# Performance work log

Hardware: AMD Instinct MI355X
Metric: run time of the kernel (lower is better)

## Reference

```python
import jax, jax.numpy as jnp
import numpy as np
from jax import lax

HEADS = 8
DIM_HEAD = 64
NUM_LANDMARKS = 256
PINV_ITERS = 6
CONV_PAD = 33 // 2  # 16


def moore_penrose_pinv(x, iters):
    # x: [..., m, m]
    abs_x = jnp.abs(x)
    col = abs_x.sum(-1).max()
    row = abs_x.sum(-2).max()
    z = jnp.swapaxes(x, -1, -2) / (col * row)
    I = jnp.eye(x.shape[-1], dtype=x.dtype)
    for _ in range(iters):
        xz = x @ z
        z = 0.25 * (z @ (13.0 * I - xz @ (15.0 * I - xz @ (7.0 * I - xz))))
    return z


def setup_inputs() -> dict:
    key = jax.random.key(0)
    k1, k2, k3, k4, k5 = jax.random.split(key, 5)
    b, n, dim = 4, 4096, 512
    inner = HEADS * DIM_HEAD
    return {
        "x": jax.random.normal(k1, (b, n, dim), jnp.float32),
        "w_qkv": jax.random.normal(k2, (dim, 3 * inner), jnp.float32) * 0.02,
        "w_out": jax.random.normal(k3, (inner, dim), jnp.float32) * 0.02,
        "b_out": jax.random.normal(k4, (dim,), jnp.float32) * 0.02,
        "res_kernel": jax.random.normal(k5, (HEADS, 1, 33, 1), jnp.float32) * 0.1,
    }


def reference(x, w_qkv, w_out, b_out, res_kernel):
    b, n, dim = x.shape
    h, dh, m = HEADS, DIM_HEAD, NUM_LANDMARKS
    scale = dh ** -0.5
    # n chosen as a multiple of m, so the pad branch is a no-op.
    l = n // m  # tokens per landmark group

    qkv = x @ w_qkv  # [b, n, 3*h*dh]
    q, k, v = jnp.split(qkv, 3, axis=-1)
    to_heads = lambda t: t.reshape(b, n, h, dh).transpose(0, 2, 1, 3)  # [b,h,n,dh]
    q, k, v = to_heads(q), to_heads(k), to_heads(v)
    q = q * scale

    # landmarks: mean over consecutive groups of l tokens
    q_l = q.reshape(b, h, m, l, dh).sum(3) / l  # [b,h,m,dh]
    k_l = k.reshape(b, h, m, l, dh).sum(3) / l

    attn1 = jax.nn.softmax(jnp.einsum("bhnd,bhmd->bhnm", q, k_l), axis=-1)  # [b,h,n,m]
    attn2 = jax.nn.softmax(jnp.einsum("bhid,bhjd->bhij", q_l, k_l), axis=-1)  # [b,h,m,m]
    attn3 = jax.nn.softmax(jnp.einsum("bhmd,bhnd->bhmn", q_l, k), axis=-1)  # [b,h,m,n]

    attn2_pinv = moore_penrose_pinv(attn2, PINV_ITERS)
    out = (attn1 @ attn2_pinv) @ (attn3 @ v)  # [b,h,n,dh]

    # depthwise residual conv over the sequence dim (Conv2d(h, h, (33,1), groups=h))
    res = lax.conv_general_dilated(
        v, res_kernel, window_strides=(1, 1),
        padding=((CONV_PAD, CONV_PAD), (0, 0)),
        dimension_numbers=("NCHW", "OIHW", "NCHW"),
        feature_group_count=h,
    )
    out = out + res

    out = out.transpose(0, 2, 1, 3).reshape(b, n, h * dh)
    out = out @ w_out + b_out
    return out
```

## Files before the change

### kernel.cpp

```cpp
#include <hip/hip_runtime.h>

#define Nq   4096
#define DHq  64
#define Mq   256
#define BHq  32

using bf16 = __bf16;
using bf16x8 = __bf16 __attribute__((ext_vector_type(8)));
using bf16x4 = __bf16 __attribute__((ext_vector_type(4)));
using f32x4 = float __attribute__((ext_vector_type(4)));

__device__ __forceinline__ f32x4 mfma16(bf16x8 a, bf16x8 b, f32x4 c) {
  return __builtin_amdgcn_mfma_f32_16x16x32_bf16(a, b, c, 0, 0, 0);
}
__device__ __forceinline__ unsigned short f2bu(float f) {
  bf16 b = (bf16)f;
  return __builtin_bit_cast(unsigned short, b);
}
__device__ __forceinline__ void split_store(bf16* h, bf16* l, long idx, float v) {
  bf16 hi = (bf16)v;
  h[idx] = hi;
  l[idx] = (bf16)(v - (float)hi);
}

typedef const __attribute__((address_space(1))) void* gas_t;
typedef __attribute__((address_space(3))) void* las_t;
__device__ __forceinline__ void glds16(const bf16* g, bf16* l) {
  __builtin_amdgcn_global_load_lds((gas_t)g, (las_t)l, 16, 0, 0);
}

template<int ROWS, int SRC>
__device__ __forceinline__ void stageA(const void* src, long ld, long row0, int k0,
                                       bf16* dst, int t) {
#pragma unroll
  for (int c = 0; c < ROWS / 64; ++c) {
    int idx = t + 256 * c;
    int r = idx >> 2;
    int kc = (idx & 3) << 3;
    bf16x8 val;
    if constexpr (SRC == 0) {
      val = *(const bf16x8*)((const bf16*)src + (row0 + r) * ld + k0 + kc);
    } else {
      const float* s = (const float*)src + (row0 + r) * ld + k0 + kc;
      float4 a = *(const float4*)s;
      float4 b = *(const float4*)(s + 4);
      val[0]=(bf16)a.x; val[1]=(bf16)a.y; val[2]=(bf16)a.z; val[3]=(bf16)a.w;
      val[4]=(bf16)b.x; val[5]=(bf16)b.y; val[6]=(bf16)b.z; val[7]=(bf16)b.w;
    }
    *(bf16x8*)(dst + r * 40 + kc) = val;
  }
}

template<int COLS, bool F32>
__device__ __forceinline__ void stageBN(const void* src, long ld, long n0, int k0,
                                        unsigned int* dst, int t) {
  int kp = t >> 4;
  int nb = (t & 15) << 2;
#pragma unroll
  for (int g = 0; g < COLS / 64; ++g) {
    int n = nb + (g << 6);
    unsigned int w0, w1, w2, w3;
    if constexpr (F32) {
      const float* s0 = (const float*)src + (long)(k0 + 2 * kp) * ld + n0 + n;
      const float* s1 = s0 + ld;
      float4 a = *(const float4*)s0;
      float4 b = *(const float4*)s1;
      w0 = f2bu(a.x) | ((unsigned)f2bu(b.x) << 16);
      w1 = f2bu(a.y) | ((unsigned)f2bu(b.y) << 16);
      w2 = f2bu(a.z) | ((unsigned)f2bu(b.z) << 16);
      w3 = f2bu(a.w) | ((unsigned)f2bu(b.w) << 16);
    } else {
      const unsigned short* s0 = (const unsigned short*)src + (long)(k0 + 2 * kp) * ld + n0 + n;
      const unsigned short* s1 = s0 + ld;
      ushort4 a = *(const ushort4*)s0;
      ushort4 b = *(const ushort4*)s1;
      w0 = a.x | ((unsigned)b.x << 16);
      w1 = a.y | ((unsigned)b.y << 16);
      w2 = a.z | ((unsigned)b.z << 16);
      w3 = a.w | ((unsigned)b.w << 16);
    }
    dst[(n + 0) * 20 + kp] = w0;
    dst[(n + 1) * 20 + kp] = w1;
    dst[(n + 2) * 20 + kp] = w2;
    dst[(n + 3) * 20 + kp] = w3;
  }
}

#define EQKV 0
#define EA2 1
#define EWT 8
#define EBIAS 9

struct GP {
  const void* A; const void* Al;
  const void* B; const void* Bl;
  long ldA, ldB, sA, sB;
  int K;
  void* C0; void* C1; void* C2;
  long sC, ldC;
  const void* x0; const void* x1;
  const float* bias;
};

template<int BM, int BN, int WX, int ASRC, int BMODE, int SPLIT, int EPI, int SWZ>
__global__ __launch_bounds__(256, 2) void mgemm(GP p) {
  constexpr int WY = 4 / WX;
  constexpr int TM = BM / WY, TN = BN / WX;
  constexpr int IT = TM / 16, JT = TN / 16;
  constexpr int AB = (SPLIT ? 2 : 1) * BM * 80;
  constexpr int BB = (SPLIT ? 2 : 1) * BN * 80;
  __shared__ __align__(16) char Lbuf[AB + BB];
  bf16* AsL = (bf16*)Lbuf;
  unsigned int* BsL = (unsigned int*)(Lbuf + AB);
  int t = threadIdx.x;
  int wv = t >> 6, lane = t & 63;
  int wy = wv / WX, wx = wv % WX;
  int qd = lane >> 4, lm = lane & 15;
  long bz = blockIdx.z, m0 = (long)blockIdx.y * BM, n0 = (long)blockIdx.x * BN;

  const void* Ap = (const bf16*)p.A + bz * p.sA;
  const void* Alp = nullptr;
  if constexpr (SPLIT) Alp = (const bf16*)p.Al + bz * p.sA;
  const void* Bp = (const bf16*)p.B + bz * p.sB;
  const void* Blp = nullptr;
  if constexpr (SPLIT) Blp = (const bf16*)p.Bl + bz * p.sB;

  f32x4 acc[IT][JT];
#pragma unroll
  for (int i = 0; i < IT; ++i)
#pragma unroll
    for (int j = 0; j < JT; ++j) acc[i][j] = (f32x4)0.0f;

  for (int k0 = 0; k0 < p.K; k0 += 32) {
    stageA<BM, ASRC>(Ap, p.ldA, m0, k0, AsL, t);
    if constexpr (SPLIT) stageA<BM, 0>(Alp, p.ldA, m0, k0, AsL + BM * 40, t);
    if constexpr (BMODE == 0) {
      stageA<BN, 0>(Bp, p.ldB, n0, k0, (bf16*)BsL, t);
      if constexpr (SPLIT) stageA<BN, 0>(Blp, p.ldB, n0, k0, (bf16*)BsL + BN * 40, t);
    } else {
      stageBN<BN, false>(Bp, p.ldB, n0, k0, BsL, t);
      if constexpr (SPLIT) stageBN<BN, false>(Blp, p.ldB, n0, k0, BsL + BN * 20, t);
    }
    __syncthreads();
    bf16x8 af[IT], afl[IT];
#pragma unroll
    for (int i = 0; i < IT; ++i) {
      int m = wy * TM + i * 16 + lm;
      af[i] = *(const bf16x8*)(AsL + m * 40 + qd * 8);
      if constexpr (SPLIT) afl[i] = *(const bf16x8*)(AsL + BM * 40 + m * 40 + qd * 8);
    }
#pragma unroll
    for (int j = 0; j < JT; ++j) {
      int n = wx * TN + j * 16 + lm;
      bf16x8 bf, bfl;
      if constexpr (BMODE == 0) {
        bf = *(const bf16x8*)((const bf16*)BsL + n * 40 + qd * 8);
        if constexpr (SPLIT) bfl = *(const bf16x8*)((const bf16*)BsL + BN * 40 + n * 40 + qd * 8);
      } else {
        bf = *(const bf16x8*)((const bf16*)(BsL + n * 20 + qd * 4));
        if constexpr (SPLIT) bfl = *(const bf16x8*)((const bf16*)(BsL + BN * 20 + n * 20 + qd * 4));
      }
#pragma unroll
      for (int i = 0; i < IT; ++i) {
        acc[i][j] = mfma16(af[i], bf, acc[i][j]);
        if constexpr (SPLIT) {
          acc[i][j] = mfma16(af[i], bfl, acc[i][j]);
          acc[i][j] = mfma16(afl[i], bf, acc[i][j]);
        }
      }
    }
    __syncthreads();
  }

  if constexpr (EPI == EA2) {
#pragma unroll
    for (int r = 0; r < 4; ++r) {
      long row = m0 + wy * TM + qd * 4 + r;
      float e[JT];
      float s = 0.f;
#pragma unroll
      for (int j = 0; j < JT; ++j) { e[j] = __expf(acc[0][j][r]); s += e[j]; }
      s += __shfl_xor(s, 1); s += __shfl_xor(s, 2);
      s += __shfl_xor(s, 4); s += __shfl_xor(s, 8);
      float inv = 1.0f / s;
#pragma unroll
      for (int j = 0; j < JT; ++j) {
        long col = n0 + j * 16 + lm;
        split_store((bf16*)p.C0, (bf16*)p.C1, bz * p.sC + row * p.ldC + col, e[j] * inv);
      }
    }
  } else {
#pragma unroll
    for (int i = 0; i < IT; ++i)
#pragma unroll
      for (int j = 0; j < JT; ++j)
#pragma unroll
        for (int r = 0; r < 4; ++r) {
          long row = m0 + wy * TM + i * 16 + qd * 4 + r;
          long col = n0 + wx * TN + j * 16 + lm;
          float v = acc[i][j][r];
          if constexpr (EPI == EWT) {
            ((bf16*)p.C0)[bz * 16384 + col * 256 + row] = (bf16)v;
          }
        }
  }
}

template<int ASRC, int EPI, int SWZ>
__global__ __launch_bounds__(256, 3) void ggemm(GP p) {
  __shared__ __align__(64) bf16 AsL[2][128 * 32];
  __shared__ __align__(64) bf16 BsL[2][128 * 32];
  int t = threadIdx.x, wv = t >> 6, lane = t & 63;
  int wy = wv >> 1, wx = wv & 1;
  int qd = lane >> 4, lm = lane & 15;
  long m0, n0;
  if constexpr (SWZ == 1) {
    int b = blockIdx.x, xcd = b & 7, s = b >> 3;
    m0 = (long)(xcd * 16 + s / 12) * 128; n0 = (long)(s % 12) * 128;
  } else {
    int b = blockIdx.x, xcd = b & 7, s = b >> 3;
    m0 = (long)(xcd * 16 + (s >> 2)) * 128; n0 = (long)(s & 3) * 128;
  }
  const bf16* A = (const bf16*)p.A;
  const bf16* B = (const bf16*)p.B;

  f32x4 acc[4][4];
#pragma unroll
  for (int i = 0; i < 4; ++i)
#pragma unroll
    for (int j = 0; j < 4; ++j) acc[i][j] = (f32x4)0.0f;

  int rsub = lane >> 2;
  int kc = (lane & 3) << 3;
  for (int k0 = 0; k0 < p.K; k0 += 64) {
#pragma unroll
    for (int half = 0; half < 2; ++half) {
      int kk = k0 + half * 32;
#pragma unroll
      for (int e = 0; e < 2; ++e) {
        int br = wv * 32 + e * 16;
        long rA = m0 + br + rsub;
        const bf16* gA;
        if constexpr (ASRC == 0) {
          gA = A + rA * p.ldA + kk + kc;
        } else {
          long bb = rA >> 12, ii = rA & 4095;
          int k = kk + kc;
          long h = k >> 6, d = k & 63;
          gA = A + (((bb * 8 + h) * 4096 + ii) * 64 + d);
        }
        glds16(gA, AsL[half] + br * 32);
        const bf16* gB = B + (n0 + br + rsub) * p.ldB + kk + kc;
        glds16(gB, BsL[half] + br * 32);
      }
    }
    __syncthreads();
#pragma unroll
    for (int half = 0; half < 2; ++half) {
      bf16x8 af[4];
#pragma unroll
      for (int i = 0; i < 4; ++i)
        af[i] = *(const bf16x8*)(AsL[half] + (wy * 64 + i * 16 + lm) * 32 + qd * 8);
#pragma unroll
      for (int j = 0; j < 4; ++j) {
        bf16x8 bv = *(const bf16x8*)(BsL[half] + (wx * 64 + j * 16 + lm) * 32 + qd * 8);
#pragma unroll
        for (int i = 0; i < 4; ++i) acc[i][j] = mfma16(af[i], bv, acc[i][j]);
      }
    }
    __syncthreads();
  }

#pragma unroll
  for (int i = 0; i < 4; ++i)
#pragma unroll
    for (int j = 0; j < 4; ++j)
#pragma unroll
      for (int r = 0; r < 4; ++r) {
        long row = m0 + wy * 64 + i * 16 + qd * 4 + r;
        long col = n0 + wx * 64 + j * 16 + lm;
        float v = acc[i][j][r];
        if constexpr (EPI == EQKV) {
          int part = (int)(col >> 9);
          long h = (col >> 6) & 7, d = col & 63;
          long bb = row >> 12, ii = row & 4095;
          float scv = part == 0 ? 0.125f : 1.0f;
          bf16* dst = part == 0 ? (bf16*)p.C0 : (part == 1 ? (bf16*)p.C1 : (bf16*)p.C2);
          dst[((bb * 8 + h) * 4096 + ii) * 64 + d] = (bf16)(v * scv);
        } else {
          ((float*)p.C0)[row * 512 + col] = v + p.bias[col];
        }
      }
}

__global__ __launch_bounds__(256) void k_prep(const float* __restrict__ x,
                                              bf16* __restrict__ xb,
                                              float* a3vf, float* rs3, unsigned int* sc) {
  long i = (long)blockIdx.x * 256 + threadIdx.x;
  long e = i * 8;
  float4 a = *(const float4*)(x + e);
  float4 b = *(const float4*)(x + e + 4);
  bf16x8 v;
  v[0]=(bf16)a.x; v[1]=(bf16)a.y; v[2]=(bf16)a.z; v[3]=(bf16)a.w;
  v[4]=(bf16)b.x; v[5]=(bf16)b.y; v[6]=(bf16)b.z; v[7]=(bf16)b.w;
  *(bf16x8*)(xb + e) = v;
  if (i < 524288) a3vf[i] = 0.f;
  if (i < 8192) rs3[i] = 0.f;
  if (i == 0) sc[0] = 0u;
}

__global__ __launch_bounds__(256) void k_wtrans2(const float* __restrict__ wq,
                                                 const float* __restrict__ wo,
                                                 bf16* __restrict__ wqt,
                                                 bf16* __restrict__ wot) {
  __shared__ float T[64][65];
  int bx = blockIdx.x, ti = blockIdx.y;
  const float* src; bf16* dst; int N, tj;
  if (bx < 24) { src = wq; dst = wqt; N = 1536; tj = bx; }
  else         { src = wo; dst = wot; N = 512;  tj = bx - 24; }
  int t = threadIdx.x;
  int c = t & 63, r0 = t >> 6;
#pragma unroll
  for (int rr = 0; rr < 16; ++rr) {
    int r = r0 * 16 + rr;
    T[r][c] = src[(long)(ti * 64 + r) * N + tj * 64 + c];
  }
  __syncthreads();
#pragma unroll
  for (int rr = 0; rr < 16; ++rr) {
    int n = r0 * 16 + rr;
    dst[(long)(tj * 64 + n) * 512 + ti * 64 + c] = (bf16)T[c][n];
  }
}

#define SBW 132

__device__ __forceinline__ void stageBS32(const bf16* src, long n0, int k0,
                                          unsigned int* dst, int t) {
  int kp = t >> 3, nb = (t & 7) << 2;
  const unsigned short* s0 = (const unsigned short*)src + (long)(k0 + 2 * kp) * 256 + n0 + nb;
  const unsigned short* s1 = s0 + 256;
  ushort4 a = *(const ushort4*)s0;
  ushort4 b = *(const ushort4*)s1;
  int wb = (k0 >> 1) + kp;
  dst[(nb + 0) * SBW + wb] = a.x | ((unsigned)b.x << 16);
  dst[(nb + 1) * SBW + wb] = a.y | ((unsigned)b.y << 16);
  dst[(nb + 2) * SBW + wb] = a.z | ((unsigned)b.z << 16);
  dst[(nb + 3) * SBW + wb] = a.w | ((unsigned)b.w << 16);
}

template<int SPLIT>
__device__ __forceinline__ void sgemm32(const bf16* Ah, const bf16* Al,
                                        const unsigned int* Bs, const unsigned int* Bsl,
                                        int w, int lane, f32x4 acc[2]) {
  int qd = lane >> 4, lm = lane & 15;
  acc[0] = (f32x4)0.0f;
  acc[1] = (f32x4)0.0f;
#pragma unroll 2
  for (int k0 = 0; k0 < 256; k0 += 32) {
    long m = w * 16 + lm;
    bf16x8 af = *(const bf16x8*)(Ah + m * 256 + k0 + qd * 8);
    bf16x8 afl;
    if constexpr (SPLIT) afl = *(const bf16x8*)(Al + m * 256 + k0 + qd * 8);
#pragma unroll
    for (int j = 0; j < 2; ++j) {
      bf16x8 bv = *(const bf16x8*)((const bf16*)(Bs + (j * 16 + lm) * SBW + (k0 >> 1) + qd * 4));
      acc[j] = mfma16(af, bv, acc[j]);
      if constexpr (SPLIT) {
        bf16x8 bl = *(const bf16x8*)((const bf16*)(Bsl + (j * 16 + lm) * SBW + (k0 >> 1) + qd * 4));
        acc[j] = mfma16(af, bl, acc[j]);
        acc[j] = mfma16(afl, bv, acc[j]);
      }
    }
  }
}

template<int HASL>
__device__ __forceinline__ void packStrip(unsigned int* Sh, unsigned int* Sl,
                                          int col, int R0, const float* v) {
  unsigned int* Wp = Sh + col * SBW + (R0 >> 1);
  Wp[0] = f2bu(v[0]) | ((unsigned)f2bu(v[1]) << 16);
  Wp[1] = f2bu(v[2]) | ((unsigned)f2bu(v[3]) << 16);
  if constexpr (HASL) {
    unsigned int* Wq = Sl + col * SBW + (R0 >> 1);
    Wq[0] = f2bu(v[0] - (float)(bf16)v[0]) | ((unsigned)f2bu(v[1] - (float)(bf16)v[1]) << 16);
    Wq[1] = f2bu(v[2] - (float)(bf16)v[2]) | ((unsigned)f2bu(v[3] - (float)(bf16)v[3]) << 16);
  }
}

__device__ __forceinline__ void nsmap(int b, long& bh, long& js) {
  int xcd = b & 7, s = b >> 3;
  bh = xcd * 4 + (s >> 3);
  js = (long)(s & 7) * 32;
}

__global__ __launch_bounds__(1024) void k_nsy0(const bf16* __restrict__ A2h,
                                               const bf16* __restrict__ zh,
                                               bf16* __restrict__ yh, bf16* __restrict__ yl) {
  __shared__ __align__(16) unsigned int Bs[32 * SBW];
  int b = blockIdx.x, t = threadIdx.x;
  long bh, js;
  nsmap(b, bh, js);
  const bf16* Ah = A2h + bh * 65536;
  const bf16* Bz = zh + bh * 65536;
  if (t < 128) {
#pragma unroll
    for (int k0 = 0; k0 < 256; k0 += 32) stageBS32(Bz, js, k0, Bs, t);
  }
  __syncthreads();
  int w = t >> 6, lane = t & 63, qd = lane >> 4, lm = lane & 15;
  f32x4 acc[2];
  sgemm32<0>(Ah, Ah, Bs, Bs, w, lane, acc);
  bf16* yhb = yh + bh * 65536;
  bf16* ylb = yl + bh * 65536;
#pragma unroll
  for (int j = 0; j < 2; ++j)
#pragma unroll
    for (int r = 0; r < 4; ++r) {
      long row = w * 16 + qd * 4 + r;
      long col = js + j * 16 + lm;
      split_store(yhb, ylb, row * 256 + col, acc[j][r]);
    }
}

template<int SPLIT, int YS>
__global__ __launch_bounds__(1024) void k_ns4(
    const bf16* __restrict__ A2h, const bf16* __restrict__ A2l,
    const bf16* __restrict__ yih, const bf16* __restrict__ yil,
    const bf16* __restrict__ zh_, const bf16* __restrict__ zl_,
    bf16* __restrict__ znh_, bf16* __restrict__ znl_,
    bf16* __restrict__ yoh_, bf16* __restrict__ yol_) {
  constexpr int P0 = SPLIT ? 2 : 1;
  constexpr int P1 = (SPLIT || YS == 1) ? 2 : 1;
  __shared__ __align__(16) unsigned int S0[P0][32 * SBW];
  __shared__ __align__(16) unsigned int S1[P1][32 * SBW];
  int b = blockIdx.x, t = threadIdx.x;
  long bh, js;
  nsmap(b, bh, js);
  const bf16* yH = yih + bh * 65536;
  const bf16* yL = yil + bh * 65536;
  const bf16* zH = zh_ + bh * 65536;
  const bf16* zL = zl_ + bh * 65536;
  const bf16* aH = A2h + bh * 65536;
  const bf16* aL = A2l + bh * 65536;
  unsigned int* S0l = S0[P0 - 1];
  unsigned int* S1l = S1[P1 - 1];
  if (t < 128) {
#pragma unroll
    for (int k0 = 0; k0 < 256; k0 += 32) {
      stageBS32(yH, js, k0, S0[0], t);
      if constexpr (SPLIT) stageBS32(yL, js, k0, S0l, t);
    }
  }
  __syncthreads();
  int w = t >> 6, lane = t & 63, qd = lane >> 4, lm = lane & 15;
  f32x4 acc[2];

  sgemm32<SPLIT>(yH, yL, S0[0], S0l, w, lane, acc);
#pragma unroll
  for (int j = 0; j < 2; ++j) {
    int R0 = w * 16 + qd * 4;
    int col = j * 16 + lm;
    float v[4];
#pragma unroll
    for (int r = 0; r < 4; ++r) {
      long row = R0 + r;
      long ix = row * 256 + js + col;
      float yv = (float)yH[ix] + (float)yL[ix];
      v[r] = ((row == js + col) ? 15.0f : 0.0f) - 7.0f * yv + acc[j][r];
    }
    packStrip<SPLIT>(S1[0], S1l, col, R0, v);
  }
  __syncthreads();

  sgemm32<SPLIT>(yH, yL, S1[0], S1l, w, lane, acc);
#pragma unroll
  for (int j = 0; j < 2; ++j) {
    int R0 = w * 16 + qd * 4;
    int col = j * 16 + lm;
    float v[4];
#pragma unroll
    for (int r = 0; r < 4; ++r)
      v[r] = (((long)(R0 + r) == js + col) ? 13.0f : 0.0f) - acc[j][r];
    packStrip<SPLIT>(S0[0], S0l, col, R0, v);
  }
  __syncthreads();

  sgemm32<SPLIT>(zH, zL, S0[0], S0l, w, lane, acc);
  bf16* zoh = znh_ + bh * 65536;
  bf16* zol = znl_ + bh * 65536;
#pragma unroll
  for (int j = 0; j < 2; ++j) {
    int R0 = w * 16 + qd * 4;
    int col = j * 16 + lm;
    float v[4];
#pragma unroll
    for (int r = 0; r < 4; ++r) {
      v[r] = 0.25f * acc[j][r];
      split_store(zoh, zol, (long)(R0 + r) * 256 + js + col, v[r]);
    }
    if constexpr (YS >= 0) packStrip<(YS == 1) ? 1 : 0>(S1[0], S1l, col, R0, v);
  }

  if constexpr (YS >= 0) {
    __syncthreads();
    sgemm32<(YS == 1) ? 1 : 0>(aH, aL, S1[0], S1l, w, lane, acc);
    bf16* yoh = yoh_ + bh * 65536;
    bf16* yol = yol_ + bh * 65536;
#pragma unroll
    for (int j = 0; j < 2; ++j)
#pragma unroll
      for (int r = 0; r < 4; ++r) {
        long row = w * 16 + qd * 4 + r;
        long col = js + j * 16 + lm;
        split_store(yoh, yol, row * 256 + col, acc[j][r]);
      }
  }
}

__device__ __forceinline__ void loadKrow4(const bf16* ks_, int t, bf16x8 kr[4]) {
#pragma unroll
  for (int c = 0; c < 4; ++c) {
    int idx = t + 256 * c;
    int r = idx >> 3, dc = (idx & 7) * 8;
    kr[c] = *(const bf16x8*)(ks_ + r * 64 + dc);
  }
}
__device__ __forceinline__ void writeKrow4(bf16* kS, int t, const bf16x8 kr[4]) {
#pragma unroll
  for (int c = 0; c < 4; ++c) {
    int idx = t + 256 * c;
    int r = idx >> 3, dc = (idx & 7) * 8;
    *(bf16x8*)(kS + r * 72 + dc) = kr[c];
  }
}
__device__ __forceinline__ void loadVhalf(const bf16* vs_, int k0, int t,
                                          ushort4& a, ushort4& b) {
  int kp = t >> 4, nb = (t & 15) << 2;
  const unsigned short* s0 = (const unsigned short*)vs_ + (long)(k0 + 2 * kp) * 64 + nb;
  a = *(const ushort4*)s0;
  b = *(const ushort4*)(s0 + 64);
}
__device__ __forceinline__ void writeVhalf(unsigned int* dst, int t, ushort4 a, ushort4 b) {
  int kp = t >> 4, nb = (t & 15) << 2;
  dst[(nb + 0) * 20 + kp] = a.x | ((unsigned)b.x << 16);
  dst[(nb + 1) * 20 + kp] = a.y | ((unsigned)b.y << 16);
  dst[(nb + 2) * 20 + kp] = a.z | ((unsigned)b.z << 16);
  dst[(nb + 3) * 20 + kp] = a.w | ((unsigned)b.w << 16);
}

__global__ __launch_bounds__(256, 2) void k_a3v(const bf16* __restrict__ qlh,
                                                const bf16* __restrict__ kb,
                                                const bf16* __restrict__ vb,
                                                float* __restrict__ a3vf,
                                                float* __restrict__ rs3) {
  __shared__ __align__(16) char L[66048];
  bf16* qlS = (bf16*)L;
  bf16* kS  = (bf16*)(L + 9216);
  bf16* PA  = (bf16*)(L + 27648);
  unsigned int* vBb = (unsigned int*)(L + 45056);
  float* rsL = (float*)(L + 65536);
  int b = blockIdx.x, t = threadIdx.x;
  int xcd = b & 7, s = b >> 3;
  int strip = xcd * 16 + (s >> 2);
  int qt = s & 3;
  long bz = strip >> 2;
  int kt = strip & 3;
  int wv = t >> 6, lane = t & 63, qd = lane >> 4, lm = lane & 15;
  int wy = wv >> 1, wx = wv & 1;
  const bf16* qlp = qlh + bz * 16384 + qt * 64 * 64;
#pragma unroll
  for (int c = 0; c < 2; ++c) {
    int idx = t + 256 * c;
    int r = idx >> 3, dc = (idx & 7) * 8;
    *(bf16x8*)(qlS + r * 72 + dc) = *(const bf16x8*)(qlp + r * 64 + dc);
  }
  const bf16* kb_ = kb + bz * 262144 + (long)kt * 65536;
  const bf16* vb_ = vb + bz * 262144 + (long)kt * 65536;
  f32x4 accO[2][2];
  float rsum[2][4];
#pragma unroll
  for (int i = 0; i < 2; ++i) {
#pragma unroll
    for (int j = 0; j < 2; ++j) accO[i][j] = (f32x4)0.0f;
#pragma unroll
    for (int r = 0; r < 4; ++r) rsum[i][r] = 0.f;
  }
  bf16x8 kr[4];
  ushort4 va[4], vbq[4];
  loadKrow4(kb_, t, kr);
#pragma unroll
  for (int q = 0; q < 4; ++q) loadVhalf(vb_, q * 32, t, va[q], vbq[q]);
  for (int tt = 0; tt < 8; ++tt) {
    __syncthreads();
    writeKrow4(kS, t, kr);
#pragma unroll
    for (int q = 0; q < 4; ++q) writeVhalf(vBb + q * 1280, t, va[q], vbq[q]);
    __syncthreads();
    if (tt < 7) {
      const bf16* ks2 = kb_ + (tt + 1) * 8192;
      const bf16* vs2 = vb_ + (tt + 1) * 8192;
      loadKrow4(ks2, t, kr);
#pragma unroll
      for (int q = 0; q < 4; ++q) loadVhalf(vs2, q * 32, t, va[q], vbq[q]);
    }
    f32x4 s2[2][4];
#pragma unroll
    for (int i = 0; i < 2; ++i)
#pragma unroll
      for (int j = 0; j < 4; ++j) s2[i][j] = (f32x4)0.0f;
#pragma unroll
    for (int ks = 0; ks < 2; ++ks) {
      bf16x8 af[2];
#pragma unroll
      for (int i = 0; i < 2; ++i)
        af[i] = *(const bf16x8*)(qlS + (wy * 32 + i * 16 + lm) * 72 + ks * 32 + qd * 8);
#pragma unroll
      for (int j = 0; j < 4; ++j) {
        bf16x8 bfv = *(const bf16x8*)(kS + (wx * 64 + j * 16 + lm) * 72 + ks * 32 + qd * 8);
#pragma unroll
        for (int i = 0; i < 2; ++i) s2[i][j] = mfma16(af[i], bfv, s2[i][j]);
      }
    }
#pragma unroll
    for (int i = 0; i < 2; ++i)
#pragma unroll
      for (int r = 0; r < 4; ++r) {
        int row = wy * 32 + i * 16 + qd * 4 + r;
        float cs = 0.f;
#pragma unroll
        for (int j = 0; j < 4; ++j) {
          float e = __expf(s2[i][j][r]);
          PA[row * 136 + wx * 64 + j * 16 + lm] = (bf16)e;
          cs += e;
        }
        cs += __shfl_xor(cs, 1); cs += __shfl_xor(cs, 2);
        cs += __shfl_xor(cs, 4); cs += __shfl_xor(cs, 8);
        rsum[i][r] += cs;
      }
    __syncthreads();
#pragma unroll
    for (int ks = 0; ks < 4; ++ks) {
      const unsigned int* vB = vBb + ks * 1280;
      bf16x8 af[2];
#pragma unroll
      for (int i = 0; i < 2; ++i)
        af[i] = *(const bf16x8*)(PA + (wy * 32 + i * 16 + lm) * 136 + ks * 32 + qd * 8);
#pragma unroll
      for (int j = 0; j < 2; ++j) {
        bf16x8 bfv = *(const bf16x8*)((const bf16*)(vB + (wx * 32 + j * 16 + lm) * 20) + qd * 8);
#pragma unroll
        for (int i = 0; i < 2; ++i) accO[i][j] = mfma16(af[i], bfv, accO[i][j]);
      }
    }
  }
  if (lm == 0) {
#pragma unroll
    for (int i = 0; i < 2; ++i)
#pragma unroll
      for (int r = 0; r < 4; ++r)
        rsL[(wy * 32 + i * 16 + qd * 4 + r) * 2 + wx] = rsum[i][r];
  }
  __syncthreads();
  if (t < 64) atomicAdd(&rs3[bz * 256 + qt * 64 + t], rsL[t * 2] + rsL[t * 2 + 1]);
#pragma unroll
  for (int i = 0; i < 2; ++i)
#pragma unroll
    for (int j = 0; j < 2; ++j)
#pragma unroll
      for (int r = 0; r < 4; ++r) {
        long row = bz * 256 + qt * 64 + wy * 32 + i * 16 + qd * 4 + r;
        long col = wx * 32 + j * 16 + lm;
        atomicAdd(&a3vf[row * 64 + col], accO[i][j][r]);
      }
}

__global__ void k_a3vnorm(const float* __restrict__ a3vf, const float* __restrict__ rs3,
                          bf16* __restrict__ a3vh, bf16* __restrict__ a3vl) {
  long e0 = ((long)blockIdx.x * 256 + threadIdx.x) * 4;
  float4 vv = *(const float4*)&a3vf[e0];
  float inv = 1.0f / rs3[e0 >> 6];
  split_store(a3vh, a3vl, e0 + 0, vv.x * inv);
  split_store(a3vh, a3vl, e0 + 1, vv.y * inv);
  split_store(a3vh, a3vl, e0 + 2, vv.z * inv);
  split_store(a3vh, a3vl, e0 + 3, vv.w * inv);
}

__global__ void k_landmarks(const bf16* q, const bf16* k, bf16* qlh, bf16* qll,
                            bf16* klh, bf16* kll) {
  int bm = blockIdx.x;
  int bh = bm >> 8, mi = bm & 255;
  int d = threadIdx.x;
  const bf16* qp = q + ((long)bh * 4096 + mi * 16) * 64 + d;
  const bf16* kp = k + ((long)bh * 4096 + mi * 16) * 64 + d;
  float sq = 0.f, sk = 0.f;
#pragma unroll
  for (int tt = 0; tt < 16; ++tt) { sq += (float)qp[tt * 64]; sk += (float)kp[tt * 64]; }
  sq *= 0.0625f; sk *= 0.0625f;
  long o = (long)bh * 16384 + mi * 64 + d;
  split_store(qlh, qll, o, sq);
  split_store(klh, kll, o, sk);
}

__global__ __launch_bounds__(256) void k_colsum(const bf16* A2h, const bf16* A2l,
                                                unsigned int* sc) {
  int bh = blockIdx.x, j = threadIdx.x;
  const bf16* ph = A2h + (long)bh * 65536 + j;
  const bf16* pl = A2l + (long)bh * 65536 + j;
  float s = 0.f;
  for (int i = 0; i < 256; ++i) s += (float)ph[i * 256] + (float)pl[i * 256];
  __shared__ float red[256];
  red[j] = s; __syncthreads();
  for (int o = 128; o > 0; o >>= 1) {
    if (j < o) red[j] = fmaxf(red[j], red[j + o]);
    __syncthreads();
  }
  if (j == 0) atomicMax(sc, __float_as_uint(red[0]));
}

__global__ __launch_bounds__(256) void k_zinit(const bf16* A2h, const bf16* A2l,
                                               const unsigned int* sc, bf16* zh, bf16* zl) {
  __shared__ float T[64][65];
  int bh = blockIdx.z, ti = blockIdx.y, tj = blockIdx.x;
  int t = threadIdx.x;
  int c = t & 63, r0 = t >> 6;
  long base = (long)bh * 65536;
  float inv = 1.0f / __uint_as_float(sc[0]);
#pragma unroll
  for (int rr = 0; rr < 16; ++rr) {
    int r = r0 * 16 + rr;
    long idx = base + (long)(ti * 64 + r) * 256 + tj * 64 + c;
    T[r][c] = (float)A2h[idx] + (float)A2l[idx];
  }
  __syncthreads();
#pragma unroll
  for (int rr = 0; rr < 16; ++rr) {
    int jl = r0 * 16 + rr;
    float v = T[c][jl] * inv;
    long o = base + (long)(tj * 64 + jl) * 256 + ti * 64 + c;
    split_store(zh, zl, o, v);
  }
}

__global__ __launch_bounds__(256, 2) void k_attn1w(const bf16* qb, const bf16* klb,
                                                   const bf16* Wt, bf16* oh) {
  __shared__ __align__(16) char L[38912];
  bf16* Aq = (bf16*)L;
  bf16* Bkl = (bf16*)(L + 5120);
  bf16* Pl = (bf16*)L;
  bf16* Bw = (bf16*)(L + 33792);
  int t = threadIdx.x, wv = t >> 6, lane = t & 63;
  int qd = lane >> 4, lm = lane & 15;
  long bz = blockIdx.z;
  long m0 = (long)blockIdx.x * 64;
  const bf16* qA = qb + bz * (4096L * 64);
  const bf16* klA = klb + bz * (256L * 64);
  const bf16* WtA = Wt + bz * 16384;

  f32x4 a1[16];
#pragma unroll
  for (int j = 0; j < 16; ++j) a1[j] = (f32x4)0.0f;
  for (int k0 = 0; k0 < 64; k0 += 32) {
    stageA<64, 0>(qA, 64, m0, k0, Aq, t);
    stageA<256, 0>(klA, 64, 0, k0, Bkl, t);
    __syncthreads();
    bf16x8 af = *(const bf16x8*)(Aq + (wv * 16 + lm) * 40 + qd * 8);
#pragma unroll
    for (int j = 0; j < 16; ++j) {
      bf16x8 bf = *(const bf16x8*)(Bkl + (j * 16 + lm) * 40 + qd * 8);
      a1[j] = mfma16(af, bf, a1[j]);
    }
    __syncthreads();
  }
  float rs[4];
#pragma unroll
  for (int r = 0; r < 4; ++r) {
    int rowl = wv * 16 + qd * 4 + r;
    float ev[16];
    float s = 0.f;
#pragma unroll
    for (int j = 0; j < 16; ++j) { ev[j] = __expf(a1[j][r]); s += ev[j]; }
    s += __shfl_xor(s, 1); s += __shfl_xor(s, 2);
    s += __shfl_xor(s, 4); s += __shfl_xor(s, 8);
    rs[r] = s;
#pragma unroll
    for (int j = 0; j < 16; ++j) {
      float other = __shfl_xor(ev[j], 1);
      if ((lm & 1) == 0) {
        unsigned int w = f2bu(ev[j]) | ((unsigned)f2bu(other) << 16);
        *(unsigned int*)(Pl + rowl * 264 + j * 16 + lm) = w;
      }
    }
  }
  f32x4 a2[4];
#pragma unroll
  for (int j = 0; j < 4; ++j) a2[j] = (f32x4)0.0f;
  for (int k0 = 0; k0 < 256; k0 += 32) {
    stageA<64, 0>(WtA, 256, 0, k0, Bw, t);
    __syncthreads();
    bf16x8 af = *(const bf16x8*)(Pl + (wv * 16 + lm) * 264 + k0 + qd * 8);
#pragma unroll
    for (int j = 0; j < 4; ++j) {
      bf16x8 bf = *(const bf16x8*)(Bw + (j * 16 + lm) * 40 + qd * 8);
      a2[j] = mfma16(af, bf, a2[j]);
    }
    __syncthreads();
  }
#pragma unroll
  for (int j = 0; j < 4; ++j)
#pragma unroll
    for (int r = 0; r < 4; ++r) {
      long grow = m0 + wv * 16 + qd * 4 + r;
      long col = j * 16 + lm;
      oh[(bz * 4096 + grow) * 64 + col] = (bf16)(a2[j][r] / rs[r]);
    }
}

__global__ __launch_bounds__(256) void k_conv2(const bf16* __restrict__ v,
                                               const float* __restrict__ kern,
                                               bf16* __restrict__ oh) {
  __shared__ __align__(16) bf16 Vs[96 * 72];
  int bx = blockIdx.x;
  int bh = bx >> 6;
  int i0 = (bx & 63) * 64;
  int t = threadIdx.x;
  const bf16* vsrc = v + (long)bh * 262144;
#pragma unroll
  for (int c = 0; c < 3; ++c) {
    int idx = t + 256 * c;
    int r = idx >> 3, dc = (idx & 7) * 8;
    int grow = i0 + r - 16;
    bf16x8 val = (bf16x8)(bf16)0.0f;
    if (grow >= 0 && grow < 4096) val = *(const bf16x8*)(vsrc + (long)grow * 64 + dc);
    *(bf16x8*)(Vs + r * 72 + dc) = val;
  }
  __syncthreads();
  int dg = t & 15, rg = t >> 4;
  const float* kc = kern + (bh & 7) * 33;
  float acc[4][4] = {};
#pragma unroll
  for (int rr = 0; rr < 36; ++rr) {
    bf16x4 xv = *(const bf16x4*)(Vs + (rg * 4 + rr) * 72 + dg * 4);
    float x0 = (float)xv[0], x1 = (float)xv[1], x2 = (float)xv[2], x3 = (float)xv[3];
#pragma unroll
    for (int r = 0; r < 4; ++r) {
      int u = rr - r;
      if (u >= 0 && u < 33) {
        float kw = kc[u];
        acc[r][0] = fmaf(kw, x0, acc[r][0]);
        acc[r][1] = fmaf(kw, x1, acc[r][1]);
        acc[r][2] = fmaf(kw, x2, acc[r][2]);
        acc[r][3] = fmaf(kw, x3, acc[r][3]);
      }
    }
  }
  long base = ((long)bh * 4096 + i0 + rg * 4) * 64 + dg * 4;
#pragma unroll
  for (int r = 0; r < 4; ++r) {
    bf16x4 o = *(const bf16x4*)(oh + base + r * 64);
    bf16x4 w;
#pragma unroll
    for (int c = 0; c < 4; ++c) w[c] = (bf16)(acc[r][c] + (float)o[c]);
    *(bf16x4*)(oh + base + r * 64) = w;
  }
}

extern "C" void kernel_launch(void* const* d_in, const int* in_sizes, int n_in,
                              void* d_out, int out_size, void* d_ws, size_t ws_size,
                              hipStream_t stream) {
  const float* x     = (const float*)d_in[0];
  const float* w_qkv = (const float*)d_in[1];
  const float* w_out = (const float*)d_in[2];
  const float* b_out = (const float*)d_in[3];
  const float* res_k = (const float*)d_in[4];

  char* w = (char*)d_ws;
  bf16* qb  = (bf16*)(w);
  bf16* kb  = (bf16*)(w + 16777216);
  bf16* vb  = (bf16*)(w + 33554432);
  bf16* qlh = (bf16*)(w + 50331648);
  bf16* qll = (bf16*)(w + 51380224);
  bf16* klh = (bf16*)(w + 52428800);
  bf16* kll = (bf16*)(w + 53477376);
  bf16* A2h = (bf16*)(w + 54525952);
  bf16* A2l = (bf16*)(w + 58720256);
  bf16* zAh = (bf16*)(w + 62914560);
  bf16* zAl = (bf16*)(w + 67108864);
  bf16* zBh = (bf16*)(w + 71303168);
  bf16* zBl = (bf16*)(w + 75497472);
  bf16* yh  = (bf16*)(w + 79691776);
  bf16* yl  = (bf16*)(w + 83886080);
  bf16* wqt = (bf16*)(w + 88080384);
  bf16* wot = (bf16*)(w + 89653248);
  bf16* y2h = (bf16*)(w + 96468992);
  bf16* y2l = (bf16*)(w + 100663296);
  bf16* oh  = (bf16*)(w + 104857600);
  bf16* xb  = (bf16*)(w + 104857600);
  float* a3vf = (float*)(w + 121634816);
  bf16* a3vh = (bf16*)(w + 123731968);
  bf16* a3vl = (bf16*)(w + 124780544);
  bf16* Wt   = (bf16*)(w + 125829120);
  float* rs3 = (float*)(w + 126877696);
  unsigned int* sc  = (unsigned int*)(w + 126910464);

  k_prep<<<4096, 256, 0, stream>>>(x, xb, a3vf, rs3, sc);
  k_wtrans2<<<dim3(32, 8), 256, 0, stream>>>(w_qkv, w_out, wqt, wot);

  GP p{};
  p.A = xb; p.ldA = 512; p.B = wqt; p.ldB = 512; p.K = 512;
  p.C0 = qb; p.C1 = kb; p.C2 = vb;
  ggemm<0, EQKV, 1><<<1536, 256, 0, stream>>>(p);

  k_landmarks<<<8192, 64, 0, stream>>>(qb, kb, qlh, qll, klh, kll);

  p = GP{};
  p.A = qlh; p.Al = qll; p.ldA = 64; p.sA = 16384;
  p.B = klh; p.Bl = kll; p.ldB = 64; p.sB = 16384; p.K = 64;
  p.C0 = A2h; p.C1 = A2l; p.sC = 65536; p.ldC = 256;
  mgemm<64, 256, 1, 0, 0, 1, EA2, 0><<<dim3(1, 4, 32), 256, 0, stream>>>(p);

  k_colsum<<<32, 256, 0, stream>>>(A2h, A2l, sc);
  k_zinit<<<dim3(4, 4, 32), 256, 0, stream>>>(A2h, A2l, sc, zAh, zAl);

  k_a3v<<<512, 256, 0, stream>>>(qlh, kb, vb, a3vf, rs3);
  k_a3vnorm<<<512, 256, 0, stream>>>(a3vf, rs3, a3vh, a3vl);

  k_nsy0<<<256, 1024, 0, stream>>>(A2h, zAh, yh, yl);
  bf16 *zch = zAh, *zcl = zAl, *znh = zBh, *znl = zBl;
  bf16 *yih = yh, *yil = yl, *yoh = y2h, *yol = y2l;
  for (int it = 0; it < 6; ++it) {
    if (it < 3)
      k_ns4<0, 0><<<256, 1024, 0, stream>>>(A2h, A2l, yih, yil, zch, zcl, znh, znl, yoh, yol);
    else if (it == 3)
      k_ns4<0, 1><<<256, 1024, 0, stream>>>(A2h, A2l, yih, yil, zch, zcl, znh, znl, yoh, yol);
    else if (it == 4)
      k_ns4<1, 1><<<256, 1024, 0, stream>>>(A2h, A2l, yih, yil, zch, zcl, znh, znl, yoh, yol);
    else
      k_ns4<1, -1><<<256, 1024, 0, stream>>>(A2h, A2l, yih, yil, zch, zcl, znh, znl, yoh, yol);
    bf16* tmp;
    tmp = zch; zch = znh; znh = tmp;
    tmp = zcl; zcl = znl; znl = tmp;
    tmp = yih; yih = yoh; yoh = tmp;
    tmp = yil; yil = yol; yol = tmp;
  }

  p = GP{};
  p.A = zch; p.Al = zcl; p.ldA = 256; p.sA = 65536;
  p.B = a3vh; p.Bl = a3vl; p.ldB = 64; p.sB = 16384; p.K = 256;
  p.C0 = Wt;
  mgemm<64, 64, 2, 0, 1, 1, EWT, 0><<<dim3(1, 4, 32), 256, 0, stream>>>(p);

  k_attn1w<<<dim3(64, 1, 32), 256, 0, stream>>>(qb, klh, Wt, oh);

  k_conv2<<<2048, 256, 0, stream>>>(vb, res_k, oh);

  p = GP{};
  p.A = oh; p.ldA = 64; p.B = wot; p.ldB = 512; p.K = 512;
  p.C0 = d_out; p.bias = b_out;
  ggemm<3, EBIAS, 2><<<512, 256, 0, stream>>>(p);
}
```

Measured before the change: 422.6 us.

## Merge prep and weight-transpose kernels; prefetch full W tile in attn1w

Folds the weight transpose/convert kernel into the input-conversion prep kernel as extra blocks, removing one launch. In k_attn1w, the whole 64x256 W tile is loaded into registers at kernel start, overlapping with the first GEMM and softmax, then written once to a larger LDS buffer. This replaces the per-k-step staging loop with its eight pairs of barriers by a single barrier. Shared memory grows to about 67KB per block, which may lower occupancy below the two blocks per CU the launch bounds request, and the 8 prefetch registers add register pressure.

```diff
diff --git a/kernel.cpp b/kernel.cpp
--- a/kernel.cpp
+++ b/kernel.cpp
@@ -295,41 +295,43 @@
 
 __global__ __launch_bounds__(256) void k_prep(const float* __restrict__ x,
                                               bf16* __restrict__ xb,
-                                              float* a3vf, float* rs3, unsigned int* sc) {
-  long i = (long)blockIdx.x * 256 + threadIdx.x;
-  long e = i * 8;
-  float4 a = *(const float4*)(x + e);
-  float4 b = *(const float4*)(x + e + 4);
-  bf16x8 v;
-  v[0]=(bf16)a.x; v[1]=(bf16)a.y; v[2]=(bf16)a.z; v[3]=(bf16)a.w;
-  v[4]=(bf16)b.x; v[5]=(bf16)b.y; v[6]=(bf16)b.z; v[7]=(bf16)b.w;
-  *(bf16x8*)(xb + e) = v;
-  if (i < 524288) a3vf[i] = 0.f;
-  if (i < 8192) rs3[i] = 0.f;
-  if (i == 0) sc[0] = 0u;
-}
-
-__global__ __launch_bounds__(256) void k_wtrans2(const float* __restrict__ wq,
-                                                 const float* __restrict__ wo,
-                                                 bf16* __restrict__ wqt,
-                                                 bf16* __restrict__ wot) {
+                                              float* a3vf, float* rs3, unsigned int* sc,
+                                              const float* __restrict__ wq,
+                                              const float* __restrict__ wo,
+                                              bf16* __restrict__ wqt,
+                                              bf16* __restrict__ wot) {
   __shared__ float T[64][65];
-  int bx = blockIdx.x, ti = blockIdx.y;
-  const float* src; bf16* dst; int N, tj;
-  if (bx < 24) { src = wq; dst = wqt; N = 1536; tj = bx; }
-  else         { src = wo; dst = wot; N = 512;  tj = bx - 24; }
-  int t = threadIdx.x;
-  int c = t & 63, r0 = t >> 6;
-#pragma unroll
-  for (int rr = 0; rr < 16; ++rr) {
-    int r = r0 * 16 + rr;
-    T[r][c] = src[(long)(ti * 64 + r) * N + tj * 64 + c];
-  }
-  __syncthreads();
-#pragma unroll
-  for (int rr = 0; rr < 16; ++rr) {
-    int n = r0 * 16 + rr;
-    dst[(long)(tj * 64 + n) * 512 + ti * 64 + c] = (bf16)T[c][n];
+  int bid = blockIdx.x, t = threadIdx.x;
+  if (bid < 4096) {
+    long i = (long)bid * 256 + t;
+    long e = i * 8;
+    float4 a = *(const float4*)(x + e);
+    float4 b = *(const float4*)(x + e + 4);
+    bf16x8 v;
+    v[0]=(bf16)a.x; v[1]=(bf16)a.y; v[2]=(bf16)a.z; v[3]=(bf16)a.w;
+    v[4]=(bf16)b.x; v[5]=(bf16)b.y; v[6]=(bf16)b.z; v[7]=(bf16)b.w;
+    *(bf16x8*)(xb + e) = v;
+    if (i < 524288) a3vf[i] = 0.f;
+    if (i < 8192) rs3[i] = 0.f;
+    if (i == 0) sc[0] = 0u;
+  } else {
+    int w = bid - 4096;
+    int bx = w >> 3, ti = w & 7;
+    const float* src; bf16* dst; int N, tj;
+    if (bx < 24) { src = wq; dst = wqt; N = 1536; tj = bx; }
+    else         { src = wo; dst = wot; N = 512;  tj = bx - 24; }
+    int c = t & 63, r0 = t >> 6;
+#pragma unroll
+    for (int rr = 0; rr < 16; ++rr) {
+      int r = r0 * 16 + rr;
+      T[r][c] = src[(long)(ti * 64 + r) * N + tj * 64 + c];
+    }
+    __syncthreads();
+#pragma unroll
+    for (int rr = 0; rr < 16; ++rr) {
+      int n = r0 * 16 + rr;
+      dst[(long)(tj * 64 + n) * 512 + ti * 64 + c] = (bf16)T[c][n];
+    }
   }
 }
 
@@ -744,11 +746,11 @@
 
 __global__ __launch_bounds__(256, 2) void k_attn1w(const bf16* qb, const bf16* klb,
                                                    const bf16* Wt, bf16* oh) {
-  __shared__ __align__(16) char L[38912];
+  __shared__ __align__(16) char L[68608];
   bf16* Aq = (bf16*)L;
   bf16* Bkl = (bf16*)(L + 5120);
   bf16* Pl = (bf16*)L;
-  bf16* Bw = (bf16*)(L + 33792);
+  bf16* Bw2 = (bf16*)(L + 33792);
   int t = threadIdx.x, wv = t >> 6, lane = t & 63;
   int qd = lane >> 4, lm = lane & 15;
   long bz = blockIdx.z;
@@ -757,6 +759,14 @@
   const bf16* klA = klb + bz * (256L * 64);
   const bf16* WtA = Wt + bz * 16384;
 
+  bf16x8 wreg[8];
+#pragma unroll
+  for (int c = 0; c < 8; ++c) {
+    int idx = t + 256 * c;
+    int r = idx >> 5, kc = (idx & 31) * 8;
+    wreg[c] = *(const bf16x8*)(WtA + r * 256 + kc);
+  }
+
   f32x4 a1[16];
 #pragma unroll
   for (int j = 0; j < 16; ++j) a1[j] = (f32x4)0.0f;
@@ -792,20 +802,28 @@
       }
     }
   }
+#pragma unroll
+  for (int c = 0; c < 8; ++c) {
+    int idx = t + 256 * c;
+    int r = idx >> 5, kc = (idx & 31) * 8;
+    int ch = kc >> 7, kk = kc & 127;
+    *(bf16x8*)(Bw2 + ch * 8704 + r * 136 + kk) = wreg[c];
+  }
+  __syncthreads();
   f32x4 a2[4];
 #pragma unroll
   for (int j = 0; j < 4; ++j) a2[j] = (f32x4)0.0f;
-  for (int k0 = 0; k0 < 256; k0 += 32) {
-    stageA<64, 0>(WtA, 256, 0, k0, Bw, t);
-    __syncthreads();
-    bf16x8 af = *(const bf16x8*)(Pl + (wv * 16 + lm) * 264 + k0 + qd * 8);
-#pragma unroll
-    for (int j = 0; j < 4; ++j) {
-      bf16x8 bf = *(const bf16x8*)(Bw + (j * 16 + lm) * 40 + qd * 8);
-      a2[j] = mfma16(af, bf, a2[j]);
-    }
-    __syncthreads();
-  }
+#pragma unroll
+  for (int ch = 0; ch < 2; ++ch)
+#pragma unroll
+    for (int k0 = 0; k0 < 128; k0 += 32) {
+      bf16x8 af = *(const bf16x8*)(Pl + (wv * 16 + lm) * 264 + ch * 128 + k0 + qd * 8);
+#pragma unroll
+      for (int j = 0; j < 4; ++j) {
+        bf16x8 bf = *(const bf16x8*)(Bw2 + ch * 8704 + (j * 16 + lm) * 136 + k0 + qd * 8);
+        a2[j] = mfma16(af, bf, a2[j]);
+      }
+    }
 #pragma unroll
   for (int j = 0; j < 4; ++j)
 #pragma unroll
@@ -903,8 +921,7 @@
   float* rs3 = (float*)(w + 126877696);
   unsigned int* sc  = (unsigned int*)(w + 126910464);
 
-  k_prep<<<4096, 256, 0, stream>>>(x, xb, a3vf, rs3, sc);
-  k_wtrans2<<<dim3(32, 8), 256, 0, stream>>>(w_qkv, w_out, wqt, wot);
+  k_prep<<<4352, 256, 0, stream>>>(x, xb, a3vf, rs3, sc, w_qkv, w_out, wqt, wot);
 
   GP p{};
   p.A = xb; p.ldA = 512; p.B = wqt; p.ldB = 512; p.K = 512;
```

New measurement: 427.2 us. Within noise of the previous version (+1.1%).
